# Kernel optimization log

Measured on AMD Instinct MI355X. Metric: run time of the kernel, lower is better.

## Reference

```python
import jax, jax.numpy as jnp
import numpy as np

TOPK = 2  # from init_kwargs


def setup_inputs() -> dict:
    key = jax.random.key(0)
    ks = jax.random.split(key, 6)
    B, T, H, S, r, ad = 2, 4096, 2048, 32, 16, 32
    h = jax.random.normal(ks[0], (B, T, H), dtype=jnp.float32)
    Wr = jax.random.normal(ks[1], (S, H), dtype=jnp.float32) * 0.02
    U = jax.random.normal(ks[2], (S, H, r), dtype=jnp.float32) * 0.02
    V = jax.random.normal(ks[3], (S, r, H), dtype=jnp.float32) * 0.02
    attr = jax.random.normal(ks[4], (S, ad), dtype=jnp.float32) * 0.02
    Wa = jax.random.normal(ks[5], (1, ad), dtype=jnp.float32) * 0.02
    return {"h": h, "Wr": Wr, "U": U, "V": V, "attr": attr, "Wa": Wa}


def reference(h, Wr, U, V, attr, Wa):
    S = Wr.shape[0]
    sc = jnp.einsum('bth,sh->bts', h, Wr)                      # router logits (B,T,S)
    _, idx = jax.lax.top_k(sc, TOPK)                           # (B,T,topk)
    m = jax.nn.one_hot(idx, S, dtype=sc.dtype).sum(axis=-2)    # topk mask (B,T,S)
    g = jax.nn.softmax(sc, axis=-1) * m
    g = g / (g.sum(axis=-1, keepdims=True) + 1e-8)
    # dense all-schema low-rank transform; fuse gate+V to avoid (B,T,S,H) buffer
    hU = jnp.einsum('bth,shr->btsr', h, U)                     # (B,T,S,r)
    out = jnp.einsum('bts,btsr,srh->bth', g, hU, V)            # (B,T,H)
    aw = jax.nn.sigmoid(attr @ Wa[0])                          # (S,)
    gate = (g @ aw)[..., None]                                 # (B,T,1)
    return out * (0.9 + 0.2 * gate)
```

## Files before the change

kernel.cpp:

```cpp
#include <hip/hip_runtime.h>
#include <cstddef>

#define BT   8192
#define HD   2048
#define NS   32
#define RDIM 16
#define AD   32
#define CAP  2048


__global__ void k_zero(int* __restrict__ cnt) {
    if (threadIdx.x < 64) cnt[threadIdx.x] = 0;
}

__global__ __launch_bounds__(256, 2) void k_router(
    const float* __restrict__ h, const float* __restrict__ Wr,
    const float* __restrict__ attr, const float* __restrict__ Wa,
    int* __restrict__ cnt, int* __restrict__ tok_list, float* __restrict__ cf_list)
{
    __shared__ float red[4][64][33];
    __shared__ float sc[8][33];
    const int tid = threadIdx.x;
    const int w = tid >> 6, L = tid & 63;
    const int t0 = blockIdx.x * 8;

    #pragma unroll 1
    for (int g = 0; g < 2; ++g) {
        const int sbase = w * 8 + g * 4;
        float acc[8][4];
        #pragma unroll
        for (int t = 0; t < 8; ++t)
            #pragma unroll
            for (int c = 0; c < 4; ++c) acc[t][c] = 0.f;

        #pragma unroll 1
        for (int i = 0; i < 8; ++i) {
            const int j = 4 * L + 256 * i;
            const float4 wv0 = *(const float4*)(Wr + (size_t)(sbase + 0) * HD + j);
            const float4 wv1 = *(const float4*)(Wr + (size_t)(sbase + 1) * HD + j);
            const float4 wv2 = *(const float4*)(Wr + (size_t)(sbase + 2) * HD + j);
            const float4 wv3 = *(const float4*)(Wr + (size_t)(sbase + 3) * HD + j);
            #pragma unroll
            for (int t = 0; t < 8; ++t) {
                const float4 hv = *(const float4*)(h + (size_t)(t0 + t) * HD + j);
                acc[t][0] += hv.x*wv0.x + hv.y*wv0.y + hv.z*wv0.z + hv.w*wv0.w;
                acc[t][1] += hv.x*wv1.x + hv.y*wv1.y + hv.z*wv1.z + hv.w*wv1.w;
                acc[t][2] += hv.x*wv2.x + hv.y*wv2.y + hv.z*wv2.z + hv.w*wv2.w;
                acc[t][3] += hv.x*wv3.x + hv.y*wv3.y + hv.z*wv3.z + hv.w*wv3.w;
            }
        }
        #pragma unroll
        for (int t = 0; t < 8; ++t)
            #pragma unroll
            for (int c = 0; c < 4; ++c)
                red[w][L][t * 4 + c] = acc[t][c];
        __syncthreads();
        if (L < 32) {
            float ssum = 0.f;
            #pragma unroll 1
            for (int k2 = 0; k2 < 64; ++k2) ssum += red[w][k2][L];
            sc[L >> 2][sbase + (L & 3)] = ssum;
        }
        __syncthreads();
    }

    if (tid < 8) {
        const int t = tid;
        float m1 = -1e30f, m2 = -1e30f;
        int i1 = 0, i2 = 0;
        #pragma unroll 1
        for (int sI = 0; sI < NS; ++sI) {
            const float v = sc[t][sI];
            if (v > m1) { m2 = m1; i2 = i1; m1 = v; i1 = sI; }
            else if (v > m2) { m2 = v; i2 = sI; }
        }
        float Z = 0.f;
        #pragma unroll 1
        for (int sI = 0; sI < NS; ++sI) Z += __expf(sc[t][sI] - m1);
        const float e2  = __expf(m2 - m1);
        const float den = 1.f + e2 + 1e-8f * Z;
        const float G1 = 1.f / den, G2 = e2 / den;
        float d1 = 0.f, d2 = 0.f;
        #pragma unroll 1
        for (int d = 0; d < AD; ++d) {
            d1 += attr[i1 * AD + d] * Wa[d];
            d2 += attr[i2 * AD + d] * Wa[d];
        }
        const float aw1 = 1.f / (1.f + __expf(-d1));
        const float aw2 = 1.f / (1.f + __expf(-d2));
        const float mult = 0.9f + 0.2f * (G1 * aw1 + G2 * aw2);
        const float c1 = G1 * mult, c2 = G2 * mult;
        const int gt = t0 + t;
        int p = atomicAdd(cnt + i1, 1);
        if (p < CAP) { tok_list[i1 * CAP + p] = gt; cf_list[i1 * CAP + p] = c1; }
        p = atomicAdd(cnt + NS + i2, 1);
        if (p < CAP) { tok_list[(NS + i2) * CAP + p] = gt; cf_list[(NS + i2) * CAP + p] = c2; }
    }
}

__global__ __launch_bounds__(256, 2) void k_expert(
    const float* __restrict__ h, const float* __restrict__ U, const float* __restrict__ V,
    const int* __restrict__ cnt, const int* __restrict__ tok_list,
    const float* __restrict__ cf_list, float* __restrict__ out, const int slot)
{
    __shared__ float smem[16 * 257 + 4096];
    __shared__ float ylds[16 * 16];
    __shared__ int   toks_s[16];
    __shared__ float cfs_s[16];

    const int tid = threadIdx.x;
    const int s = blockIdx.x;
    const int base = slot * NS + s;
    int count = cnt[base];
    if (count > CAP) count = CAP;

    float* hs = smem;
    float* us = smem + 16 * 257;

    const int slot4 = tid & 15, jsub = tid >> 4;
    const int tg = slot4 >> 2, kq = slot4 & 3;
    const int w = tid >> 6, L = tid & 63;
    const int tg2 = tid >> 5, jg = tid & 31;

    #pragma unroll 1
    for (int ci = blockIdx.y; ci * 16 < count; ci += gridDim.y) {
        const int nt = min(16, count - ci * 16);
        if (tid < 16) {
            if (tid < nt) {
                toks_s[tid] = tok_list[base * CAP + ci * 16 + tid];
                cfs_s[tid]  = cf_list[base * CAP + ci * 16 + tid];
            } else { toks_s[tid] = 0; cfs_s[tid] = 0.f; }
        }
        __syncthreads();

        float acc[4][4];
        #pragma unroll
        for (int a = 0; a < 4; ++a)
            #pragma unroll
            for (int b = 0; b < 4; ++b) acc[a][b] = 0.f;

        #pragma unroll 1
        for (int c = 0; c < 8; ++c) {
            #pragma unroll
            for (int rr = 0; rr < 4; ++rr) {
                const int row = w * 4 + rr;
                float4 hv = {0.f, 0.f, 0.f, 0.f};
                if (row < nt)
                    hv = *(const float4*)(h + (size_t)toks_s[row] * HD + c * 256 + L * 4);
                float* hp = hs + row * 257 + L * 4;
                hp[0] = hv.x; hp[1] = hv.y; hp[2] = hv.z; hp[3] = hv.w;
            }
            const float* Up = U + ((size_t)s * HD + c * 256) * RDIM;
            #pragma unroll
            for (int q = 0; q < 4; ++q)
                *(float4*)(us + (q * 256 + tid) * 4) = *(const float4*)(Up + (q * 256 + tid) * 4);
            __syncthreads();

            const int j0 = jsub * 16;
            #pragma unroll
            for (int jj = 0; jj < 16; ++jj) {
                const float4 uv = *(const float4*)(us + (j0 + jj) * 16 + kq * 4);
                #pragma unroll
                for (int tt = 0; tt < 4; ++tt) {
                    const float hv = hs[(tg * 4 + tt) * 257 + j0 + jj];
                    acc[tt][0] += hv * uv.x;
                    acc[tt][1] += hv * uv.y;
                    acc[tt][2] += hv * uv.z;
                    acc[tt][3] += hv * uv.w;
                }
            }
            __syncthreads();
        }

        float* yp = smem;
        #pragma unroll
        for (int m = 0; m < 16; ++m)
            yp[tid * 17 + m] = acc[m >> 2][m & 3];
        __syncthreads();
        {
            const int t = tid >> 4, k = tid & 15;
            const int sl = (t >> 2) * 4 + (k >> 2);
            const int m  = (t & 3) * 4 + (k & 3);
            float yv = 0.f;
            #pragma unroll
            for (int js = 0; js < 16; ++js)
                yv += yp[(js * 16 + sl) * 17 + m];
            ylds[t * 16 + k] = yv * cfs_s[t];
        }
        __syncthreads();

        float yr[2][16];
        #pragma unroll
        for (int tt = 0; tt < 2; ++tt)
            #pragma unroll
            for (int k = 0; k < 16; ++k)
                yr[tt][k] = ylds[(tg2 * 2 + tt) * 16 + k];

        float* vs = smem;
        #pragma unroll 1
        for (int c = 0; c < 8; ++c) {
            const float* Vp = V + (size_t)s * RDIM * HD + c * 256;
            #pragma unroll
            for (int rr = 0; rr < 4; ++rr) {
                const int k = w * 4 + rr;
                *(float4*)(vs + k * 260 + L * 4) = *(const float4*)(Vp + (size_t)k * HD + L * 4);
            }
            __syncthreads();

            float a0[2][4], a1[2][4];
            #pragma unroll
            for (int tt = 0; tt < 2; ++tt)
                #pragma unroll
                for (int u = 0; u < 4; ++u) { a0[tt][u] = 0.f; a1[tt][u] = 0.f; }
            #pragma unroll
            for (int k = 0; k < 16; ++k) {
                const float4 v0 = *(const float4*)(vs + k * 260 + jg * 8);
                const float4 v1 = *(const float4*)(vs + k * 260 + jg * 8 + 4);
                #pragma unroll
                for (int tt = 0; tt < 2; ++tt) {
                    const float f = yr[tt][k];
                    a0[tt][0] += f * v0.x; a0[tt][1] += f * v0.y;
                    a0[tt][2] += f * v0.z; a0[tt][3] += f * v0.w;
                    a1[tt][0] += f * v1.x; a1[tt][1] += f * v1.y;
                    a1[tt][2] += f * v1.z; a1[tt][3] += f * v1.w;
                }
            }
            #pragma unroll
            for (int tt = 0; tt < 2; ++tt) {
                const int row = tg2 * 2 + tt;
                if (row < nt) {
                    float* op = out + (size_t)toks_s[row] * HD + c * 256 + jg * 8;
                    if (slot == 0) {
                        *(float4*)(op)     = make_float4(a0[tt][0], a0[tt][1], a0[tt][2], a0[tt][3]);
                        *(float4*)(op + 4) = make_float4(a1[tt][0], a1[tt][1], a1[tt][2], a1[tt][3]);
                    } else {
                        float4 o0 = *(const float4*)(op);
                        float4 o1 = *(const float4*)(op + 4);
                        o0.x += a0[tt][0]; o0.y += a0[tt][1]; o0.z += a0[tt][2]; o0.w += a0[tt][3];
                        o1.x += a1[tt][0]; o1.y += a1[tt][1]; o1.z += a1[tt][2]; o1.w += a1[tt][3];
                        *(float4*)(op)     = o0;
                        *(float4*)(op + 4) = o1;
                    }
                }
            }
            __syncthreads();
        }
    }
}

extern "C" void kernel_launch(void* const* d_in, const int* in_sizes, int n_in,
                              void* d_out, int out_size, void* d_ws, size_t ws_size,
                              hipStream_t stream)
{
    const float* h    = (const float*)d_in[0];
    const float* Wr   = (const float*)d_in[1];
    const float* U    = (const float*)d_in[2];
    const float* V    = (const float*)d_in[3];
    const float* attr = (const float*)d_in[4];
    const float* Wa   = (const float*)d_in[5];
    float* out = (float*)d_out;

    int*   cnt      = (int*)d_ws;
    int*   tok_list = (int*)((char*)d_ws + 256);
    float* cf_list  = (float*)((char*)d_ws + 256 + (size_t)64 * CAP * sizeof(int));

    hipLaunchKernelGGL(k_zero,   dim3(1),          dim3(64),  0, stream, cnt);
    hipLaunchKernelGGL(k_router, dim3(BT / 8),     dim3(256), 0, stream,
                       h, Wr, attr, Wa, cnt, tok_list, cf_list);
    hipLaunchKernelGGL(k_expert, dim3(NS, 32),     dim3(256), 0, stream,
                       h, U, V, cnt, tok_list, cf_list, out, 0);
    hipLaunchKernelGGL(k_expert, dim3(NS, 32),     dim3(256), 0, stream,
                       h, U, V, cnt, tok_list, cf_list, out, 1);
}
```

Measured before the change: 322.4 us.

## Double-buffer router and expert kernels with direct global-to-LDS loads

The router now handles 32 tokens per block instead of 8, staging h through double-buffered LDS with global_load_lds so each Wr load is reused across more tokens. The expert kernel double-buffers h and U chunks, transposes U in LDS for dot4-style inner products, and prefetches V tiles the same way. Each thread now writes four float4 output segments per row, and the grid's y dimension drops from 32 to 24. The aim is to hide global-load latency and cut redundant Wr and h traffic, at the cost of more LDS per block and possibly lower occupancy.

```diff
diff --git a/kernel.cpp b/kernel.cpp
--- a/kernel.cpp
+++ b/kernel.cpp
@@ -1,5 +1,6 @@
 #include <hip/hip_runtime.h>
 #include <cstddef>
+#include <cstdint>
 
 #define BT   8192
 #define HD   2048
@@ -8,75 +9,95 @@
 #define AD   32
 #define CAP  2048
 
+#define RT_M 32
+#define EX_T 16
+#define HPAD 260
+
+__device__ __forceinline__ void gld16(const float* g, float* l) {
+    __builtin_amdgcn_global_load_lds(
+        (const __attribute__((address_space(1))) unsigned int*)g,
+        (__attribute__((address_space(3))) unsigned int*)l, 16, 0, 0);
+}
+
+__device__ __forceinline__ float dot4(const float4 a, const float4 b) {
+    return a.x * b.x + a.y * b.y + a.z * b.z + a.w * b.w;
+}
+__device__ __forceinline__ void fma4(float4& o, const float a, const float4 b) {
+    o.x += a * b.x; o.y += a * b.y; o.z += a * b.z; o.w += a * b.w;
+}
 
 __global__ void k_zero(int* __restrict__ cnt) {
     if (threadIdx.x < 64) cnt[threadIdx.x] = 0;
 }
 
-__global__ __launch_bounds__(256, 2) void k_router(
+__global__ __launch_bounds__(256) void k_router(
     const float* __restrict__ h, const float* __restrict__ Wr,
     const float* __restrict__ attr, const float* __restrict__ Wa,
     int* __restrict__ cnt, int* __restrict__ tok_list, float* __restrict__ cf_list)
 {
-    __shared__ float red[4][64][33];
-    __shared__ float sc[8][33];
-    const int tid = threadIdx.x;
-    const int w = tid >> 6, L = tid & 63;
-    const int t0 = blockIdx.x * 8;
+    __shared__ float hbuf[2][RT_M][HPAD];
+    __shared__ float sc_s[RT_M][NS + 1];
+
+    const int tid  = threadIdx.x;
+    const int w    = tid >> 6, lane = tid & 63;
+    const int tp   = tid >> 4;
+    const int sp   = tid & 15;
+    const int t0   = blockIdx.x * RT_M;
+
+    #pragma unroll
+    for (int r = 0; r < 8; ++r) {
+        const int row = w * 8 + r;
+        gld16(h + (size_t)(t0 + row) * HD + lane * 4, &hbuf[0][row][0]);
+    }
+    __syncthreads();
+
+    float a00 = 0.f, a01 = 0.f, a10 = 0.f, a11 = 0.f;
 
     #pragma unroll 1
-    for (int g = 0; g < 2; ++g) {
-        const int sbase = w * 8 + g * 4;
-        float acc[8][4];
-        #pragma unroll
-        for (int t = 0; t < 8; ++t)
-            #pragma unroll
-            for (int c = 0; c < 4; ++c) acc[t][c] = 0.f;
-
-        #pragma unroll 1
-        for (int i = 0; i < 8; ++i) {
-            const int j = 4 * L + 256 * i;
-            const float4 wv0 = *(const float4*)(Wr + (size_t)(sbase + 0) * HD + j);
-            const float4 wv1 = *(const float4*)(Wr + (size_t)(sbase + 1) * HD + j);
-            const float4 wv2 = *(const float4*)(Wr + (size_t)(sbase + 2) * HD + j);
-            const float4 wv3 = *(const float4*)(Wr + (size_t)(sbase + 3) * HD + j);
-            #pragma unroll
-            for (int t = 0; t < 8; ++t) {
-                const float4 hv = *(const float4*)(h + (size_t)(t0 + t) * HD + j);
-                acc[t][0] += hv.x*wv0.x + hv.y*wv0.y + hv.z*wv0.z + hv.w*wv0.w;
-                acc[t][1] += hv.x*wv1.x + hv.y*wv1.y + hv.z*wv1.z + hv.w*wv1.w;
-                acc[t][2] += hv.x*wv2.x + hv.y*wv2.y + hv.z*wv2.z + hv.w*wv2.w;
-                acc[t][3] += hv.x*wv3.x + hv.y*wv3.y + hv.z*wv3.z + hv.w*wv3.w;
-            }
-        }
-        #pragma unroll
-        for (int t = 0; t < 8; ++t)
-            #pragma unroll
-            for (int c = 0; c < 4; ++c)
-                red[w][L][t * 4 + c] = acc[t][c];
-        __syncthreads();
-        if (L < 32) {
-            float ssum = 0.f;
-            #pragma unroll 1
-            for (int k2 = 0; k2 < 64; ++k2) ssum += red[w][k2][L];
-            sc[L >> 2][sbase + (L & 3)] = ssum;
+    for (int c = 0; c < 8; ++c) {
+        if (c < 7) {
+            #pragma unroll
+            for (int r = 0; r < 8; ++r) {
+                const int row = w * 8 + r;
+                gld16(h + (size_t)(t0 + row) * HD + (c + 1) * 256 + lane * 4,
+                      &hbuf[(c + 1) & 1][row][0]);
+            }
+        }
+        const float4* h0 = (const float4*)&hbuf[c & 1][2 * tp][0];
+        const float4* h1 = (const float4*)&hbuf[c & 1][2 * tp + 1][0];
+        const float4* w0 = (const float4*)(Wr + (size_t)(2 * sp) * HD + c * 256);
+        const float4* w1 = (const float4*)(Wr + (size_t)(2 * sp + 1) * HD + c * 256);
+        #pragma unroll 4
+        for (int jq = 0; jq < 64; ++jq) {
+            const float4 hv0 = h0[jq], hv1 = h1[jq];
+            const float4 wv0 = w0[jq], wv1 = w1[jq];
+            a00 += dot4(hv0, wv0);
+            a01 += dot4(hv0, wv1);
+            a10 += dot4(hv1, wv0);
+            a11 += dot4(hv1, wv1);
         }
         __syncthreads();
     }
 
-    if (tid < 8) {
+    sc_s[2 * tp    ][2 * sp    ] = a00;
+    sc_s[2 * tp    ][2 * sp + 1] = a01;
+    sc_s[2 * tp + 1][2 * sp    ] = a10;
+    sc_s[2 * tp + 1][2 * sp + 1] = a11;
+    __syncthreads();
+
+    if (tid < RT_M) {
         const int t = tid;
         float m1 = -1e30f, m2 = -1e30f;
         int i1 = 0, i2 = 0;
         #pragma unroll 1
         for (int sI = 0; sI < NS; ++sI) {
-            const float v = sc[t][sI];
+            const float v = sc_s[t][sI];
             if (v > m1) { m2 = m1; i2 = i1; m1 = v; i1 = sI; }
             else if (v > m2) { m2 = v; i2 = sI; }
         }
         float Z = 0.f;
         #pragma unroll 1
-        for (int sI = 0; sI < NS; ++sI) Z += __expf(sc[t][sI] - m1);
+        for (int sI = 0; sI < NS; ++sI) Z += __expf(sc_s[t][sI] - m1);
         const float e2  = __expf(m2 - m1);
         const float den = 1.f + e2 + 1e-8f * Z;
         const float G1 = 1.f / den, G2 = e2 / den;
@@ -98,41 +119,61 @@
     }
 }
 
-__global__ __launch_bounds__(256, 2) void k_expert(
+__global__ __launch_bounds__(256) void k_expert(
     const float* __restrict__ h, const float* __restrict__ U, const float* __restrict__ V,
     const int* __restrict__ cnt, const int* __restrict__ tok_list,
     const float* __restrict__ cf_list, float* __restrict__ out, const int slot)
 {
-    __shared__ float smem[16 * 257 + 4096];
-    __shared__ float ylds[16 * 16];
-    __shared__ int   toks_s[16];
-    __shared__ float cfs_s[16];
+    __shared__ float hb[2][EX_T][HPAD];
+    __shared__ float ub[2][RDIM][HPAD];
+    __shared__ float ylds[EX_T][RDIM + 1];
+    __shared__ int   toks_s[EX_T];
+    __shared__ float cfs_s[EX_T];
 
     const int tid = threadIdx.x;
     const int s = blockIdx.x;
     const int base = slot * NS + s;
-    int count = cnt[base];
-    if (count > CAP) count = CAP;
-
-    float* hs = smem;
-    float* us = smem + 16 * 257;
-
-    const int slot4 = tid & 15, jsub = tid >> 4;
-    const int tg = slot4 >> 2, kq = slot4 & 3;
-    const int w = tid >> 6, L = tid & 63;
-    const int tg2 = tid >> 5, jg = tid & 31;
+    int count = cnt[base]; if (count > CAP) count = CAP;
+
+    const int w = tid >> 6, lane = tid & 63;
+    const int tg = w;
+    const int kg = (tid >> 4) & 3;
+    const int js = tid & 15;
+    const int jgrp = tid >> 2, qq = tid & 3;
+    const int tB = tid >> 4, jg = tid & 15;
+
+    const float* Ubase = U + (size_t)s * HD * RDIM;
+    const float* Vbase = V + (size_t)s * RDIM * HD;
 
     #pragma unroll 1
-    for (int ci = blockIdx.y; ci * 16 < count; ci += gridDim.y) {
-        const int nt = min(16, count - ci * 16);
-        if (tid < 16) {
+    for (int ci = blockIdx.y; ci * EX_T < count; ci += gridDim.y) {
+        const int nt = min(EX_T, count - ci * EX_T);
+        if (tid < EX_T) {
             if (tid < nt) {
-                toks_s[tid] = tok_list[base * CAP + ci * 16 + tid];
-                cfs_s[tid]  = cf_list[base * CAP + ci * 16 + tid];
+                toks_s[tid] = tok_list[base * CAP + ci * EX_T + tid];
+                cfs_s[tid]  = cf_list[base * CAP + ci * EX_T + tid];
             } else { toks_s[tid] = 0; cfs_s[tid] = 0.f; }
         }
         __syncthreads();
 
+        #pragma unroll
+        for (int r = 0; r < 4; ++r) {
+            const int row = tg * 4 + r;
+            gld16(h + (size_t)toks_s[row] * HD + lane * 4, &hb[0][row][0]);
+        }
+        float4 up[4];
+        #pragma unroll
+        for (int rr = 0; rr < 4; ++rr)
+            up[rr] = *(const float4*)(Ubase + (size_t)(jgrp * 4 + rr) * RDIM + qq * 4);
+        #pragma unroll
+        for (int rr = 0; rr < 4; ++rr) {
+            ub[0][qq * 4 + 0][jgrp * 4 + rr] = up[rr].x;
+            ub[0][qq * 4 + 1][jgrp * 4 + rr] = up[rr].y;
+            ub[0][qq * 4 + 2][jgrp * 4 + rr] = up[rr].z;
+            ub[0][qq * 4 + 3][jgrp * 4 + rr] = up[rr].w;
+        }
+        __syncthreads();
+
         float acc[4][4];
         #pragma unroll
         for (int a = 0; a < 4; ++a)
@@ -141,107 +182,110 @@
 
         #pragma unroll 1
         for (int c = 0; c < 8; ++c) {
-            #pragma unroll
-            for (int rr = 0; rr < 4; ++rr) {
-                const int row = w * 4 + rr;
-                float4 hv = {0.f, 0.f, 0.f, 0.f};
-                if (row < nt)
-                    hv = *(const float4*)(h + (size_t)toks_s[row] * HD + c * 256 + L * 4);
-                float* hp = hs + row * 257 + L * 4;
-                hp[0] = hv.x; hp[1] = hv.y; hp[2] = hv.z; hp[3] = hv.w;
-            }
-            const float* Up = U + ((size_t)s * HD + c * 256) * RDIM;
-            #pragma unroll
-            for (int q = 0; q < 4; ++q)
-                *(float4*)(us + (q * 256 + tid) * 4) = *(const float4*)(Up + (q * 256 + tid) * 4);
+            const int cur = c & 1, nxt = cur ^ 1;
+            if (c < 7) {
+                #pragma unroll
+                for (int r = 0; r < 4; ++r) {
+                    const int row = tg * 4 + r;
+                    gld16(h + (size_t)toks_s[row] * HD + (c + 1) * 256 + lane * 4,
+                          &hb[nxt][row][0]);
+                }
+                #pragma unroll
+                for (int rr = 0; rr < 4; ++rr)
+                    up[rr] = *(const float4*)(Ubase +
+                              (size_t)((c + 1) * 256 + jgrp * 4 + rr) * RDIM + qq * 4);
+            }
+            #pragma unroll
+            for (int jq = 0; jq < 4; ++jq) {
+                const int col = js * 4 + jq * 64;
+                float4 hv0 = *(const float4*)&hb[cur][tg * 4 + 0][col];
+                float4 hv1 = *(const float4*)&hb[cur][tg * 4 + 1][col];
+                float4 hv2 = *(const float4*)&hb[cur][tg * 4 + 2][col];
+                float4 hv3 = *(const float4*)&hb[cur][tg * 4 + 3][col];
+                #pragma unroll
+                for (int kk = 0; kk < 4; ++kk) {
+                    const float4 uv = *(const float4*)&ub[cur][kg * 4 + kk][col];
+                    acc[0][kk] += dot4(hv0, uv);
+                    acc[1][kk] += dot4(hv1, uv);
+                    acc[2][kk] += dot4(hv2, uv);
+                    acc[3][kk] += dot4(hv3, uv);
+                }
+            }
+            if (c < 7) {
+                #pragma unroll
+                for (int rr = 0; rr < 4; ++rr) {
+                    ub[nxt][qq * 4 + 0][jgrp * 4 + rr] = up[rr].x;
+                    ub[nxt][qq * 4 + 1][jgrp * 4 + rr] = up[rr].y;
+                    ub[nxt][qq * 4 + 2][jgrp * 4 + rr] = up[rr].z;
+                    ub[nxt][qq * 4 + 3][jgrp * 4 + rr] = up[rr].w;
+                }
+            }
             __syncthreads();
-
-            const int j0 = jsub * 16;
-            #pragma unroll
-            for (int jj = 0; jj < 16; ++jj) {
-                const float4 uv = *(const float4*)(us + (j0 + jj) * 16 + kq * 4);
-                #pragma unroll
-                for (int tt = 0; tt < 4; ++tt) {
-                    const float hv = hs[(tg * 4 + tt) * 257 + j0 + jj];
-                    acc[tt][0] += hv * uv.x;
-                    acc[tt][1] += hv * uv.y;
-                    acc[tt][2] += hv * uv.z;
-                    acc[tt][3] += hv * uv.w;
-                }
-            }
-            __syncthreads();
-        }
-
-        float* yp = smem;
-        #pragma unroll
-        for (int m = 0; m < 16; ++m)
-            yp[tid * 17 + m] = acc[m >> 2][m & 3];
+        }
+
+        float* red = &ub[0][0][0];
+        #pragma unroll
+        for (int tt = 0; tt < 4; ++tt)
+            #pragma unroll
+            for (int kk = 0; kk < 4; ++kk)
+                red[js * HPAD + (tg * 4 + tt) * 16 + (kg * 4 + kk)] = acc[tt][kk];
         __syncthreads();
         {
             const int t = tid >> 4, k = tid & 15;
-            const int sl = (t >> 2) * 4 + (k >> 2);
-            const int m  = (t & 3) * 4 + (k & 3);
             float yv = 0.f;
             #pragma unroll
-            for (int js = 0; js < 16; ++js)
-                yv += yp[(js * 16 + sl) * 17 + m];
-            ylds[t * 16 + k] = yv * cfs_s[t];
-        }
-        __syncthreads();
-
-        float yr[2][16];
-        #pragma unroll
-        for (int tt = 0; tt < 2; ++tt)
-            #pragma unroll
-            for (int k = 0; k < 16; ++k)
-                yr[tt][k] = ylds[(tg2 * 2 + tt) * 16 + k];
-
-        float* vs = smem;
+            for (int j2 = 0; j2 < 16; ++j2) yv += red[j2 * HPAD + t * 16 + k];
+            ylds[t][k] = yv * cfs_s[t];
+        }
+        __syncthreads();
+
+        #pragma unroll
+        for (int r = 0; r < 4; ++r) {
+            const int row = tg * 4 + r;
+            gld16(Vbase + (size_t)row * HD + lane * 4, &hb[0][row][0]);
+        }
+        __syncthreads();
+
+        const bool act = tB < nt;
         #pragma unroll 1
         for (int c = 0; c < 8; ++c) {
-            const float* Vp = V + (size_t)s * RDIM * HD + c * 256;
-            #pragma unroll
-            for (int rr = 0; rr < 4; ++rr) {
-                const int k = w * 4 + rr;
-                *(float4*)(vs + k * 260 + L * 4) = *(const float4*)(Vp + (size_t)k * HD + L * 4);
-            }
-            __syncthreads();
-
-            float a0[2][4], a1[2][4];
-            #pragma unroll
-            for (int tt = 0; tt < 2; ++tt)
-                #pragma unroll
-                for (int u = 0; u < 4; ++u) { a0[tt][u] = 0.f; a1[tt][u] = 0.f; }
-            #pragma unroll
-            for (int k = 0; k < 16; ++k) {
-                const float4 v0 = *(const float4*)(vs + k * 260 + jg * 8);
-                const float4 v1 = *(const float4*)(vs + k * 260 + jg * 8 + 4);
-                #pragma unroll
-                for (int tt = 0; tt < 2; ++tt) {
-                    const float f = yr[tt][k];
-                    a0[tt][0] += f * v0.x; a0[tt][1] += f * v0.y;
-                    a0[tt][2] += f * v0.z; a0[tt][3] += f * v0.w;
-                    a1[tt][0] += f * v1.x; a1[tt][1] += f * v1.y;
-                    a1[tt][2] += f * v1.z; a1[tt][3] += f * v1.w;
-                }
-            }
-            #pragma unroll
-            for (int tt = 0; tt < 2; ++tt) {
-                const int row = tg2 * 2 + tt;
-                if (row < nt) {
-                    float* op = out + (size_t)toks_s[row] * HD + c * 256 + jg * 8;
-                    if (slot == 0) {
-                        *(float4*)(op)     = make_float4(a0[tt][0], a0[tt][1], a0[tt][2], a0[tt][3]);
-                        *(float4*)(op + 4) = make_float4(a1[tt][0], a1[tt][1], a1[tt][2], a1[tt][3]);
-                    } else {
-                        float4 o0 = *(const float4*)(op);
-                        float4 o1 = *(const float4*)(op + 4);
-                        o0.x += a0[tt][0]; o0.y += a0[tt][1]; o0.z += a0[tt][2]; o0.w += a0[tt][3];
-                        o1.x += a1[tt][0]; o1.y += a1[tt][1]; o1.z += a1[tt][2]; o1.w += a1[tt][3];
-                        *(float4*)(op)     = o0;
-                        *(float4*)(op + 4) = o1;
-                    }
-                }
+            const int cur = c & 1, nxt = cur ^ 1;
+            if (c < 7) {
+                #pragma unroll
+                for (int r = 0; r < 4; ++r) {
+                    const int row = tg * 4 + r;
+                    gld16(Vbase + (size_t)row * HD + (c + 1) * 256 + lane * 4,
+                          &hb[nxt][row][0]);
+                }
+            }
+            float* op = out + (size_t)toks_s[tB] * HD + c * 256 + jg * 4;
+            float4 ov0, ov1, ov2, ov3;
+            if (slot == 1 && act) {
+                ov0 = *(const float4*)(op);
+                ov1 = *(const float4*)(op + 64);
+                ov2 = *(const float4*)(op + 128);
+                ov3 = *(const float4*)(op + 192);
+            }
+            float4 o0 = {0,0,0,0}, o1 = {0,0,0,0}, o2 = {0,0,0,0}, o3 = {0,0,0,0};
+            #pragma unroll
+            for (int k = 0; k < RDIM; ++k) {
+                const float yv = ylds[tB][k];
+                fma4(o0, yv, *(const float4*)&hb[cur][k][jg * 4]);
+                fma4(o1, yv, *(const float4*)&hb[cur][k][jg * 4 + 64]);
+                fma4(o2, yv, *(const float4*)&hb[cur][k][jg * 4 + 128]);
+                fma4(o3, yv, *(const float4*)&hb[cur][k][jg * 4 + 192]);
+            }
+            if (act) {
+                if (slot == 1) {
+                    o0.x += ov0.x; o0.y += ov0.y; o0.z += ov0.z; o0.w += ov0.w;
+                    o1.x += ov1.x; o1.y += ov1.y; o1.z += ov1.z; o1.w += ov1.w;
+                    o2.x += ov2.x; o2.y += ov2.y; o2.z += ov2.z; o2.w += ov2.w;
+                    o3.x += ov3.x; o3.y += ov3.y; o3.z += ov3.z; o3.w += ov3.w;
+                }
+                *(float4*)(op)       = o0;
+                *(float4*)(op + 64)  = o1;
+                *(float4*)(op + 128) = o2;
+                *(float4*)(op + 192) = o3;
             }
             __syncthreads();
         }
@@ -258,17 +302,17 @@
     const float* V    = (const float*)d_in[3];
     const float* attr = (const float*)d_in[4];
     const float* Wa   = (const float*)d_in[5];
-    float* out = (float*)d_out;
+    float* outp = (float*)d_out;
 
     int*   cnt      = (int*)d_ws;
     int*   tok_list = (int*)((char*)d_ws + 256);
     float* cf_list  = (float*)((char*)d_ws + 256 + (size_t)64 * CAP * sizeof(int));
 
-    hipLaunchKernelGGL(k_zero,   dim3(1),          dim3(64),  0, stream, cnt);
-    hipLaunchKernelGGL(k_router, dim3(BT / 8),     dim3(256), 0, stream,
+    hipLaunchKernelGGL(k_zero,   dim3(1),           dim3(64),  0, stream, cnt);
+    hipLaunchKernelGGL(k_router, dim3(BT / RT_M),   dim3(256), 0, stream,
                        h, Wr, attr, Wa, cnt, tok_list, cf_list);
-    hipLaunchKernelGGL(k_expert, dim3(NS, 32),     dim3(256), 0, stream,
-                       h, U, V, cnt, tok_list, cf_list, out, 0);
-    hipLaunchKernelGGL(k_expert, dim3(NS, 32),     dim3(256), 0, stream,
-                       h, U, V, cnt, tok_list, cf_list, out, 1);
-}
+    hipLaunchKernelGGL(k_expert, dim3(NS, 24),      dim3(256), 0, stream,
+                       h, U, V, cnt, tok_list, cf_list, outp, 0);
+    hipLaunchKernelGGL(k_expert, dim3(NS, 24),      dim3(256), 0, stream,
+                       h, U, V, cnt, tok_list, cf_list, outp, 1);
+}
```

Result: slower. 434.9 us (+34.9%).

## Split expert into down/up kernels with transposed U and shuffle-reduced dot products

Applied to the files above, without the earlier changes.

A prep kernel transposes U into an [S][r][H] layout, which makes the U reads coalesced, and also zeroes the counters. The router replaces its LDS reduction with a register transpose-reduce built on wave shuffles, and double-buffers the h loads. The expert work is split in two. k_A computes y = h·U for both slots in one launch using shuffle reductions and writes y to workspace. k_B then applies V with no LDS tiling and no per-chunk barriers, reading V straight from global/L2. The change adds a workspace round trip for y, an extra launch, high register pressure (64-value accumulators), and uncoalesced V reuse that relies on the cache.

```diff
diff --git a/kernel.cpp b/kernel.cpp
--- a/kernel.cpp
+++ b/kernel.cpp
@@ -9,60 +9,91 @@
 #define CAP  2048
 
 
-__global__ void k_zero(int* __restrict__ cnt) {
-    if (threadIdx.x < 64) cnt[threadIdx.x] = 0;
-}
-
-__global__ __launch_bounds__(256, 2) void k_router(
+__device__ __forceinline__ float dot4(const float4 a, const float4 b) {
+    return a.x * b.x + a.y * b.y + a.z * b.z + a.w * b.w;
+}
+__device__ __forceinline__ void fma4(float4& o, const float a, const float4 b) {
+    o.x += a * b.x; o.y += a * b.y; o.z += a * b.z; o.w += a * b.w;
+}
+
+__global__ __launch_bounds__(256) void k_prep(const float* __restrict__ U,
+                                              int* __restrict__ cnt,
+                                              float* __restrict__ UT) {
+    const int bx = blockIdx.x;
+    if (bx == NS * 8) { if (threadIdx.x < 64) cnt[threadIdx.x] = 0; return; }
+    const int s = bx >> 3, jc = bx & 7;
+    const int j = jc * 256 + threadIdx.x;
+    const float4* Up = (const float4*)(U + ((size_t)s * HD + j) * RDIM);
+    const float4 a = Up[0], b = Up[1], c = Up[2], d = Up[3];
+    float* Tp = UT + (size_t)s * RDIM * HD + j;
+    Tp[0]       = a.x; Tp[HD]      = a.y; Tp[2*HD]   = a.z; Tp[3*HD]   = a.w;
+    Tp[4*HD]    = b.x; Tp[5*HD]    = b.y; Tp[6*HD]   = b.z; Tp[7*HD]   = b.w;
+    Tp[8*HD]    = c.x; Tp[9*HD]    = c.y; Tp[10*HD]  = c.z; Tp[11*HD]  = c.w;
+    Tp[12*HD]   = d.x; Tp[13*HD]   = d.y; Tp[14*HD]  = d.z; Tp[15*HD]  = d.w;
+}
+
+__global__ __launch_bounds__(256) void k_router(
     const float* __restrict__ h, const float* __restrict__ Wr,
     const float* __restrict__ attr, const float* __restrict__ Wa,
     int* __restrict__ cnt, int* __restrict__ tok_list, float* __restrict__ cf_list)
 {
-    __shared__ float red[4][64][33];
-    __shared__ float sc[8][33];
-    const int tid = threadIdx.x;
-    const int w = tid >> 6, L = tid & 63;
+    __shared__ float sc_s[8][NS + 1];
+    const int tid = threadIdx.x, w = tid >> 6, lane = tid & 63;
     const int t0 = blockIdx.x * 8;
 
     #pragma unroll 1
     for (int g = 0; g < 2; ++g) {
-        const int sbase = w * 8 + g * 4;
-        float acc[8][4];
+        const int sb = w * 8 + g * 4;
+        float vals[32];
+        #pragma unroll
+        for (int m = 0; m < 32; ++m) vals[m] = 0.f;
+
+        float4 hA[8], hB[8];
         #pragma unroll
         for (int t = 0; t < 8; ++t)
-            #pragma unroll
-            for (int c = 0; c < 4; ++c) acc[t][c] = 0.f;
-
-        #pragma unroll 1
-        for (int i = 0; i < 8; ++i) {
-            const int j = 4 * L + 256 * i;
-            const float4 wv0 = *(const float4*)(Wr + (size_t)(sbase + 0) * HD + j);
-            const float4 wv1 = *(const float4*)(Wr + (size_t)(sbase + 1) * HD + j);
-            const float4 wv2 = *(const float4*)(Wr + (size_t)(sbase + 2) * HD + j);
-            const float4 wv3 = *(const float4*)(Wr + (size_t)(sbase + 3) * HD + j);
-            #pragma unroll
-            for (int t = 0; t < 8; ++t) {
-                const float4 hv = *(const float4*)(h + (size_t)(t0 + t) * HD + j);
-                acc[t][0] += hv.x*wv0.x + hv.y*wv0.y + hv.z*wv0.z + hv.w*wv0.w;
-                acc[t][1] += hv.x*wv1.x + hv.y*wv1.y + hv.z*wv1.z + hv.w*wv1.w;
-                acc[t][2] += hv.x*wv2.x + hv.y*wv2.y + hv.z*wv2.z + hv.w*wv2.w;
-                acc[t][3] += hv.x*wv3.x + hv.y*wv3.y + hv.z*wv3.z + hv.w*wv3.w;
-            }
-        }
-        #pragma unroll
-        for (int t = 0; t < 8; ++t)
-            #pragma unroll
-            for (int c = 0; c < 4; ++c)
-                red[w][L][t * 4 + c] = acc[t][c];
-        __syncthreads();
-        if (L < 32) {
-            float ssum = 0.f;
-            #pragma unroll 1
-            for (int k2 = 0; k2 < 64; ++k2) ssum += red[w][k2][L];
-            sc[L >> 2][sbase + (L & 3)] = ssum;
-        }
-        __syncthreads();
+            hA[t] = *(const float4*)(h + (size_t)(t0 + t) * HD + lane * 4);
+
+        #pragma unroll 1
+        for (int c = 0; c < 8; c += 2) {
+            #pragma unroll
+            for (int t = 0; t < 8; ++t)
+                hB[t] = *(const float4*)(h + (size_t)(t0 + t) * HD + (c + 1) * 256 + lane * 4);
+            #pragma unroll
+            for (int sl = 0; sl < 4; ++sl) {
+                const float4 wv = *(const float4*)(Wr + (size_t)(sb + sl) * HD + c * 256 + lane * 4);
+                #pragma unroll
+                for (int t = 0; t < 8; ++t) vals[t * 4 + sl] += dot4(hA[t], wv);
+            }
+            if (c < 6) {
+                #pragma unroll
+                for (int t = 0; t < 8; ++t)
+                    hA[t] = *(const float4*)(h + (size_t)(t0 + t) * HD + (c + 2) * 256 + lane * 4);
+            }
+            #pragma unroll
+            for (int sl = 0; sl < 4; ++sl) {
+                const float4 wv = *(const float4*)(Wr + (size_t)(sb + sl) * HD + (c + 1) * 256 + lane * 4);
+                #pragma unroll
+                for (int t = 0; t < 8; ++t) vals[t * 4 + sl] += dot4(hB[t], wv);
+            }
+        }
+
+        #pragma unroll
+        for (int st = 0; st < 5; ++st) {
+            const int d = 1 << st;
+            const bool up = (lane & d) != 0;
+            const int half = 16 >> st;
+            #pragma unroll
+            for (int i = 0; i < half; ++i) {
+                const float lo = vals[2 * i], hi = vals[2 * i + 1];
+                const float keep = up ? hi : lo, send = up ? lo : hi;
+                vals[i] = keep + __shfl_xor(send, d, 64);
+            }
+        }
+        vals[0] += __shfl_xor(vals[0], 32, 64);
+        if (lane < 32)
+            sc_s[lane >> 2][sb + (lane & 3)] = vals[0];
     }
+    __syncthreads();
 
     if (tid < 8) {
         const int t = tid;
@@ -70,13 +101,13 @@
         int i1 = 0, i2 = 0;
         #pragma unroll 1
         for (int sI = 0; sI < NS; ++sI) {
-            const float v = sc[t][sI];
+            const float v = sc_s[t][sI];
             if (v > m1) { m2 = m1; i2 = i1; m1 = v; i1 = sI; }
             else if (v > m2) { m2 = v; i2 = sI; }
         }
         float Z = 0.f;
         #pragma unroll 1
-        for (int sI = 0; sI < NS; ++sI) Z += __expf(sc[t][sI] - m1);
+        for (int sI = 0; sI < NS; ++sI) Z += __expf(sc_s[t][sI] - m1);
         const float e2  = __expf(m2 - m1);
         const float den = 1.f + e2 + 1e-8f * Z;
         const float G1 = 1.f / den, G2 = e2 / den;
@@ -98,152 +129,150 @@
     }
 }
 
-__global__ __launch_bounds__(256, 2) void k_expert(
-    const float* __restrict__ h, const float* __restrict__ U, const float* __restrict__ V,
-    const int* __restrict__ cnt, const int* __restrict__ tok_list,
-    const float* __restrict__ cf_list, float* __restrict__ out, const int slot)
+__global__ __launch_bounds__(256) void k_A(
+    const float* __restrict__ h, const int* __restrict__ cnt,
+    const int* __restrict__ tok_list, const float* __restrict__ cf_list,
+    const float* __restrict__ UT, float* __restrict__ y_ws)
 {
-    __shared__ float smem[16 * 257 + 4096];
-    __shared__ float ylds[16 * 16];
-    __shared__ int   toks_s[16];
-    __shared__ float cfs_s[16];
-
-    const int tid = threadIdx.x;
-    const int s = blockIdx.x;
-    const int base = slot * NS + s;
-    int count = cnt[base];
-    if (count > CAP) count = CAP;
-
-    float* hs = smem;
-    float* us = smem + 16 * 257;
-
-    const int slot4 = tid & 15, jsub = tid >> 4;
-    const int tg = slot4 >> 2, kq = slot4 & 3;
-    const int w = tid >> 6, L = tid & 63;
-    const int tg2 = tid >> 5, jg = tid & 31;
+    const int g = blockIdx.x, s = g & (NS - 1);
+    int count = cnt[g]; if (count > CAP) count = CAP;
+    const int tid = threadIdx.x, w = tid >> 6, lane = tid & 63;
+    const float* UTs = UT + (size_t)s * RDIM * HD;
 
     #pragma unroll 1
     for (int ci = blockIdx.y; ci * 16 < count; ci += gridDim.y) {
-        const int nt = min(16, count - ci * 16);
-        if (tid < 16) {
-            if (tid < nt) {
-                toks_s[tid] = tok_list[base * CAP + ci * 16 + tid];
-                cfs_s[tid]  = cf_list[base * CAP + ci * 16 + tid];
-            } else { toks_s[tid] = 0; cfs_s[tid] = 0.f; }
-        }
+        int tok[4]; float cf[4];
+        #pragma unroll
+        for (int r = 0; r < 4; ++r) {
+            const int idx = ci * 16 + w * 4 + r;
+            const bool vld = idx < count;
+            tok[r] = vld ? tok_list[g * CAP + idx] : 0;
+            cf[r]  = vld ? cf_list[g * CAP + idx] : 0.f;
+        }
+
+        float vals[64];
+        #pragma unroll
+        for (int m = 0; m < 64; ++m) vals[m] = 0.f;
+
+        float4 hA[4], hB[4];
+        #pragma unroll
+        for (int r = 0; r < 4; ++r)
+            hA[r] = *(const float4*)(h + (size_t)tok[r] * HD + lane * 4);
+
+        #pragma unroll 1
+        for (int c = 0; c < 8; c += 2) {
+            #pragma unroll
+            for (int r = 0; r < 4; ++r)
+                hB[r] = *(const float4*)(h + (size_t)tok[r] * HD + (c + 1) * 256 + lane * 4);
+            #pragma unroll
+            for (int kg = 0; kg < 4; ++kg) {
+                #pragma unroll
+                for (int q = 0; q < 4; ++q) {
+                    const float4 uv = *(const float4*)(UTs + (size_t)(kg * 4 + q) * HD + c * 256 + lane * 4);
+                    #pragma unroll
+                    for (int r = 0; r < 4; ++r)
+                        vals[r * 16 + kg * 4 + q] += dot4(hA[r], uv);
+                }
+            }
+            if (c < 6) {
+                #pragma unroll
+                for (int r = 0; r < 4; ++r)
+                    hA[r] = *(const float4*)(h + (size_t)tok[r] * HD + (c + 2) * 256 + lane * 4);
+            }
+            #pragma unroll
+            for (int kg = 0; kg < 4; ++kg) {
+                #pragma unroll
+                for (int q = 0; q < 4; ++q) {
+                    const float4 uv = *(const float4*)(UTs + (size_t)(kg * 4 + q) * HD + (c + 1) * 256 + lane * 4);
+                    #pragma unroll
+                    for (int r = 0; r < 4; ++r)
+                        vals[r * 16 + kg * 4 + q] += dot4(hB[r], uv);
+                }
+            }
+        }
+
+        #pragma unroll
+        for (int st = 0; st < 6; ++st) {
+            const int d = 1 << st;
+            const bool up = (lane & d) != 0;
+            const int half = 32 >> st;
+            #pragma unroll
+            for (int i = 0; i < half; ++i) {
+                const float lo = vals[2 * i], hi = vals[2 * i + 1];
+                const float keep = up ? hi : lo, send = up ? lo : hi;
+                vals[i] = keep + __shfl_xor(send, d, 64);
+            }
+        }
+        const int rsel = lane >> 4;
+        const float cfv = rsel == 0 ? cf[0] : rsel == 1 ? cf[1] : rsel == 2 ? cf[2] : cf[3];
+        y_ws[(size_t)g * (CAP * 16) + (size_t)(ci * 16 + w * 4) * 16 + lane] = vals[0] * cfv;
+    }
+}
+
+__global__ __launch_bounds__(256) void k_B(
+    const float* __restrict__ V, const int* __restrict__ cnt,
+    const int* __restrict__ tok_list, const float* __restrict__ y_ws,
+    float* __restrict__ out, const int slot)
+{
+    __shared__ __align__(16) float ylds[256];
+    __shared__ int toks_s[16];
+    const int gsch = blockIdx.x;
+    const int g = slot * NS + gsch;
+    int count = cnt[g]; if (count > CAP) count = CAP;
+    const int tid = threadIdx.x, w = tid >> 6, lane = tid & 63;
+    const float* Vs = V + (size_t)gsch * RDIM * HD;
+
+    #pragma unroll 1
+    for (int ci = blockIdx.y; ci * 16 < count; ci += gridDim.y) {
         __syncthreads();
-
-        float acc[4][4];
-        #pragma unroll
-        for (int a = 0; a < 4; ++a)
-            #pragma unroll
-            for (int b = 0; b < 4; ++b) acc[a][b] = 0.f;
+        if (tid < 16)
+            toks_s[tid] = (ci * 16 + tid < count) ? tok_list[g * CAP + ci * 16 + tid] : -1;
+        ylds[tid] = y_ws[(size_t)g * (CAP * 16) + (size_t)ci * 256 + tid];
+        __syncthreads();
+
+        int tok[4]; bool act[4];
+        #pragma unroll
+        for (int r = 0; r < 4; ++r) {
+            const int tv = toks_s[w * 4 + r];
+            act[r] = tv >= 0; tok[r] = act[r] ? tv : 0;
+        }
 
         #pragma unroll 1
         for (int c = 0; c < 8; ++c) {
-            #pragma unroll
-            for (int rr = 0; rr < 4; ++rr) {
-                const int row = w * 4 + rr;
-                float4 hv = {0.f, 0.f, 0.f, 0.f};
-                if (row < nt)
-                    hv = *(const float4*)(h + (size_t)toks_s[row] * HD + c * 256 + L * 4);
-                float* hp = hs + row * 257 + L * 4;
-                hp[0] = hv.x; hp[1] = hv.y; hp[2] = hv.z; hp[3] = hv.w;
-            }
-            const float* Up = U + ((size_t)s * HD + c * 256) * RDIM;
-            #pragma unroll
-            for (int q = 0; q < 4; ++q)
-                *(float4*)(us + (q * 256 + tid) * 4) = *(const float4*)(Up + (q * 256 + tid) * 4);
-            __syncthreads();
-
-            const int j0 = jsub * 16;
-            #pragma unroll
-            for (int jj = 0; jj < 16; ++jj) {
-                const float4 uv = *(const float4*)(us + (j0 + jj) * 16 + kq * 4);
-                #pragma unroll
-                for (int tt = 0; tt < 4; ++tt) {
-                    const float hv = hs[(tg * 4 + tt) * 257 + j0 + jj];
-                    acc[tt][0] += hv * uv.x;
-                    acc[tt][1] += hv * uv.y;
-                    acc[tt][2] += hv * uv.z;
-                    acc[tt][3] += hv * uv.w;
+            float4 ov[4];
+            if (slot) {
+                #pragma unroll
+                for (int r = 0; r < 4; ++r)
+                    if (act[r]) ov[r] = *(const float4*)(out + (size_t)tok[r] * HD + c * 256 + lane * 4);
+            }
+            float4 o[4];
+            #pragma unroll
+            for (int r = 0; r < 4; ++r) o[r] = make_float4(0.f, 0.f, 0.f, 0.f);
+
+            #pragma unroll
+            for (int kg = 0; kg < 4; ++kg) {
+                float4 vv[4];
+                #pragma unroll
+                for (int q = 0; q < 4; ++q)
+                    vv[q] = *(const float4*)(Vs + (size_t)(kg * 4 + q) * HD + c * 256 + lane * 4);
+                #pragma unroll
+                for (int r = 0; r < 4; ++r) {
+                    const float4 yv = *(const float4*)&ylds[(w * 4 + r) * 16 + kg * 4];
+                    fma4(o[r], yv.x, vv[0]); fma4(o[r], yv.y, vv[1]);
+                    fma4(o[r], yv.z, vv[2]); fma4(o[r], yv.w, vv[3]);
                 }
             }
-            __syncthreads();
-        }
-
-        float* yp = smem;
-        #pragma unroll
-        for (int m = 0; m < 16; ++m)
-            yp[tid * 17 + m] = acc[m >> 2][m & 3];
-        __syncthreads();
-        {
-            const int t = tid >> 4, k = tid & 15;
-            const int sl = (t >> 2) * 4 + (k >> 2);
-            const int m  = (t & 3) * 4 + (k & 3);
-            float yv = 0.f;
-            #pragma unroll
-            for (int js = 0; js < 16; ++js)
-                yv += yp[(js * 16 + sl) * 17 + m];
-            ylds[t * 16 + k] = yv * cfs_s[t];
-        }
-        __syncthreads();
-
-        float yr[2][16];
-        #pragma unroll
-        for (int tt = 0; tt < 2; ++tt)
-            #pragma unroll
-            for (int k = 0; k < 16; ++k)
-                yr[tt][k] = ylds[(tg2 * 2 + tt) * 16 + k];
-
-        float* vs = smem;
-        #pragma unroll 1
-        for (int c = 0; c < 8; ++c) {
-            const float* Vp = V + (size_t)s * RDIM * HD + c * 256;
-            #pragma unroll
-            for (int rr = 0; rr < 4; ++rr) {
-                const int k = w * 4 + rr;
-                *(float4*)(vs + k * 260 + L * 4) = *(const float4*)(Vp + (size_t)k * HD + L * 4);
-            }
-            __syncthreads();
-
-            float a0[2][4], a1[2][4];
-            #pragma unroll
-            for (int tt = 0; tt < 2; ++tt)
-                #pragma unroll
-                for (int u = 0; u < 4; ++u) { a0[tt][u] = 0.f; a1[tt][u] = 0.f; }
-            #pragma unroll
-            for (int k = 0; k < 16; ++k) {
-                const float4 v0 = *(const float4*)(vs + k * 260 + jg * 8);
-                const float4 v1 = *(const float4*)(vs + k * 260 + jg * 8 + 4);
-                #pragma unroll
-                for (int tt = 0; tt < 2; ++tt) {
-                    const float f = yr[tt][k];
-                    a0[tt][0] += f * v0.x; a0[tt][1] += f * v0.y;
-                    a0[tt][2] += f * v0.z; a0[tt][3] += f * v0.w;
-                    a1[tt][0] += f * v1.x; a1[tt][1] += f * v1.y;
-                    a1[tt][2] += f * v1.z; a1[tt][3] += f * v1.w;
+            #pragma unroll
+            for (int r = 0; r < 4; ++r) {
+                if (act[r]) {
+                    float* op = out + (size_t)tok[r] * HD + c * 256 + lane * 4;
+                    if (slot) {
+                        o[r].x += ov[r].x; o[r].y += ov[r].y;
+                        o[r].z += ov[r].z; o[r].w += ov[r].w;
+                    }
+                    *(float4*)op = o[r];
                 }
             }
-            #pragma unroll
-            for (int tt = 0; tt < 2; ++tt) {
-                const int row = tg2 * 2 + tt;
-                if (row < nt) {
-                    float* op = out + (size_t)toks_s[row] * HD + c * 256 + jg * 8;
-                    if (slot == 0) {
-                        *(float4*)(op)     = make_float4(a0[tt][0], a0[tt][1], a0[tt][2], a0[tt][3]);
-                        *(float4*)(op + 4) = make_float4(a1[tt][0], a1[tt][1], a1[tt][2], a1[tt][3]);
-                    } else {
-                        float4 o0 = *(const float4*)(op);
-                        float4 o1 = *(const float4*)(op + 4);
-                        o0.x += a0[tt][0]; o0.y += a0[tt][1]; o0.z += a0[tt][2]; o0.w += a0[tt][3];
-                        o1.x += a1[tt][0]; o1.y += a1[tt][1]; o1.z += a1[tt][2]; o1.w += a1[tt][3];
-                        *(float4*)(op)     = o0;
-                        *(float4*)(op + 4) = o1;
-                    }
-                }
-            }
-            __syncthreads();
         }
     }
 }
@@ -258,17 +287,22 @@
     const float* V    = (const float*)d_in[3];
     const float* attr = (const float*)d_in[4];
     const float* Wa   = (const float*)d_in[5];
-    float* out = (float*)d_out;
-
-    int*   cnt      = (int*)d_ws;
-    int*   tok_list = (int*)((char*)d_ws + 256);
-    float* cf_list  = (float*)((char*)d_ws + 256 + (size_t)64 * CAP * sizeof(int));
-
-    hipLaunchKernelGGL(k_zero,   dim3(1),          dim3(64),  0, stream, cnt);
-    hipLaunchKernelGGL(k_router, dim3(BT / 8),     dim3(256), 0, stream,
+    float* outp = (float*)d_out;
+
+    char* ws = (char*)d_ws;
+    int*   cnt      = (int*)ws;
+    int*   tok_list = (int*)(ws + 256);
+    float* cf_list  = (float*)(ws + 256 + (size_t)64 * CAP * 4);
+    float* UT       = (float*)(ws + 256 + (size_t)2 * 64 * CAP * 4);
+    float* y_ws     = UT + (size_t)NS * RDIM * HD;
+
+    hipLaunchKernelGGL(k_prep,   dim3(NS * 8 + 1),  dim3(256), 0, stream, U, cnt, UT);
+    hipLaunchKernelGGL(k_router, dim3(BT / 8),      dim3(256), 0, stream,
                        h, Wr, attr, Wa, cnt, tok_list, cf_list);
-    hipLaunchKernelGGL(k_expert, dim3(NS, 32),     dim3(256), 0, stream,
-                       h, U, V, cnt, tok_list, cf_list, out, 0);
-    hipLaunchKernelGGL(k_expert, dim3(NS, 32),     dim3(256), 0, stream,
-                       h, U, V, cnt, tok_list, cf_list, out, 1);
-}
+    hipLaunchKernelGGL(k_A,      dim3(64, 32),      dim3(256), 0, stream,
+                       h, cnt, tok_list, cf_list, UT, y_ws);
+    hipLaunchKernelGGL(k_B,      dim3(NS, 32),      dim3(256), 0, stream,
+                       V, cnt, tok_list, y_ws, outp, 0);
+    hipLaunchKernelGGL(k_B,      dim3(NS, 32),      dim3(256), 0, stream,
+                       V, cnt, tok_list, y_ws, outp, 1);
+}
```

Measured after the change: 276.1 us. -14.4%, faster.
